# Kernel tuning notes

Hardware: AMD Instinct MI355X
Metric: run time of the kernel (lower is better)

The kernel has to match this reference:

```python
import jax, jax.numpy as jnp
import numpy as np
from jax import lax

K, C, H, W = 5, 256, 64, 64
NH, HD, P = 8, 32, 16           # heads, head_dim, patch_number
H0, W0 = 512, 512               # original mask resolution
SCALE_BASE = HD ** (-0.5)
GN_EPS = 1e-5


def _l2norm(x):
    n = jnp.sqrt(jnp.sum(x * x, axis=-1, keepdims=True))
    return x / jnp.maximum(n, 1e-12)


def _conv(x, w, b, pad):
    y = lax.conv_general_dilated(x, w, (1, 1), [(pad, pad), (pad, pad)],
                                 dimension_numbers=('NCHW', 'OIHW', 'NCHW'))
    return y + b[None, :, None, None]


def _group_norm(x, scale, bias, groups=4):
    n, c, h, w = x.shape
    xg = x.reshape(n, groups, -1)
    mu = jnp.mean(xg, axis=-1, keepdims=True)
    var = jnp.var(xg, axis=-1, keepdims=True)
    xg = (xg - mu) / jnp.sqrt(var + GN_EPS)
    return xg.reshape(n, c, h, w) * scale[None, :, None, None] + bias[None, :, None, None]


def setup_inputs() -> dict:
    key = jax.random.key(0)
    ks = jax.random.split(key, 16)
    x = jax.random.normal(ks[0], (1 + K, C, H, W), dtype=jnp.float32)
    delta = (jax.random.uniform(ks[1], (K, 1, H0, W0)) < 0.3).astype(jnp.float32)
    w = lambda k, sh: jax.random.normal(k, sh, dtype=jnp.float32) * 0.02
    return {
        'x': x, 'delta_onehot_x': delta,
        'Wq': w(ks[2], (C, C)), 'bq': jnp.zeros((C,), jnp.float32),
        'Ws': w(ks[3], (C, C)), 'bs': jnp.zeros((C,), jnp.float32),
        'scale': jnp.array(1.0, jnp.float32),
        'c1w': w(ks[4], (16, NH, 5, 5)), 'c1b': jnp.zeros((16,), jnp.float32),
        'g1s': jnp.ones((16,), jnp.float32), 'g1b': jnp.zeros((16,), jnp.float32),
        'c2w': w(ks[5], (64, 16, 3, 3)), 'c2b': jnp.zeros((64,), jnp.float32),
        'g2s': jnp.ones((64,), jnp.float32), 'g2b': jnp.zeros((64,), jnp.float32),
        'c3w': w(ks[6], (128, 64, 3, 3)), 'c3b': jnp.zeros((128,), jnp.float32),
        'g3s': jnp.ones((128,), jnp.float32), 'g3b': jnp.zeros((128,), jnp.float32),
    }


def reference(x, delta_onehot_x, Wq, bq, Ws, bs, scale,
              c1w, c1b, g1s, g1b, c2w, c2b, g2s, g2b, c3w, c3b, g3s, g3b):
    q = jnp.transpose(x[:1], (0, 2, 3, 1))    # [1,H,W,C]
    s = jnp.transpose(x[1:], (0, 2, 3, 1))    # [K,H,W,C]

    # nearest interpolation (torch 'nearest': src = floor(dst*in/out))
    ih = (jnp.arange(H) * H0) // H
    iw = (jnp.arange(W) * W0) // W
    d = delta_onehot_x[:, :, ih][:, :, :, iw]  # [K,1,H,W]

    q = (q @ Wq.T + bq).reshape(H, W, NH, HD).transpose(2, 0, 1, 3)        # [h,H,W,d]
    s = (s @ Ws.T + bs).reshape(K, H, W, NH, HD).transpose(0, 3, 1, 2, 4)  # [K,h,H,W,d]
    q = _l2norm(q) * scale * SCALE_BASE
    s = _l2norm(s)

    Hp, Wp = H // P, W // P
    S = P * P
    fg = d.reshape(K, P, Hp, P, Wp).transpose(0, 1, 3, 2, 4).reshape(K, S, Hp * Wp)
    bg = 1.0 - fg
    fg_sum = jnp.sum(fg, axis=-1)  # [K,S]
    bg_sum = jnp.sum(bg, axis=-1)

    sp = s.reshape(K, NH, P, Hp, P, Wp, HD).transpose(0, 1, 2, 4, 3, 5, 6)
    sp = sp.reshape(K, NH, S, Hp * Wp, HD)

    cs_fg = _l2norm(jnp.einsum('ksl,khsld->khsd', fg, sp))
    cs_bg = _l2norm(jnp.einsum('ksl,khsld->khsd', bg, sp))
    c_s = jnp.concatenate([cs_fg, cs_bg], axis=2).transpose(1, 0, 2, 3).reshape(NH, K * 2 * S, HD)
    c_v = jnp.concatenate([jnp.ones((K, NH, S), q.dtype), jnp.zeros((K, NH, S), q.dtype)],
                          axis=2).transpose(1, 0, 2).reshape(NH, K * 2 * S)

    mask = jnp.concatenate([jnp.where(fg_sum < 1.0, -jnp.inf, 0.0),
                            jnp.where(bg_sum < 1.0, -jnp.inf, 0.0)], axis=1)  # [K,2S]
    mask = mask.reshape(1, 1, 1, -1)

    attn = jax.nn.softmax(jnp.einsum('hyxd,hsd->hyxs', q, c_s) + mask, axis=-1)
    xo = jnp.einsum('hyxs,hs->hyx', attn, c_v)[None]  # [1,h,H,W]

    out = jax.nn.relu(_group_norm(_conv(xo, c1w, c1b, 2), g1s, g1b))
    out = jax.nn.relu(_group_norm(_conv(out, c2w, c2b, 1), g2s, g2b))
    out = jax.nn.relu(_group_norm(_conv(out, c3w, c3b, 1), g3s, g3b))
    return out
```

## Files before the change

### kernel.cpp

```cpp
#include <hip/hip_runtime.h>
#include <hip/hip_bf16.h>
#include <cstddef>

#define HW 4096

typedef __attribute__((ext_vector_type(8))) short bf16x8;
typedef __attribute__((ext_vector_type(4))) float f32x4;

__device__ __forceinline__ unsigned short f2b(float v) {
  __hip_bfloat16 b = __float2bfloat16(v);
  return *reinterpret_cast<unsigned short*>(&b);
}
__device__ __forceinline__ float b2f(unsigned short u) {
  return __bfloat162float(*reinterpret_cast<const __hip_bfloat16*>(&u));
}

__global__ __launch_bounds__(256) void txp_kernel(const float* __restrict__ x,
                                                  unsigned short* __restrict__ xb) {
  const int n = blockIdx.z, p0 = blockIdx.x * 64, ci0 = blockIdx.y * 64;
  const int t = threadIdx.x;
  __shared__ float Tl[64][65];
#pragma unroll
  for (int pass = 0; pass < 16; ++pass) {
    int ci = pass * 4 + (t >> 6), px = t & 63;
    Tl[ci][px] = x[((size_t)n * 256 + ci0 + ci) * HW + p0 + px];
  }
  __syncthreads();
#pragma unroll
  for (int pass = 0; pass < 16; ++pass) {
    int px = pass * 4 + (t >> 6), ci = t & 63;
    xb[((size_t)n * HW + p0 + px) * 256 + ci0 + ci] = f2b(Tl[ci][px]);
  }
}

__global__ __launch_bounds__(256) void wcv_kernel(const float* __restrict__ Wq,
                                                  const float* __restrict__ Ws,
                                                  unsigned short* __restrict__ wb) {
  int i = blockIdx.x * 256 + threadIdx.x;
  const float* W = (i < 65536) ? Wq : Ws;
  wb[i] = f2b(W[i & 65535]);
}

__global__ __launch_bounds__(256) void proj_kernel(
    const unsigned short* __restrict__ xb, const unsigned short* __restrict__ wb,
    const float* __restrict__ bq, const float* __restrict__ bs,
    const float* __restrict__ scale,
    unsigned short* __restrict__ qb, unsigned short* __restrict__ sb) {
  const int row0 = blockIdx.x * 128;
  const int n    = row0 >> 12;
  const int co0  = blockIdx.y * 64;
  const int t    = threadIdx.x;
  const int wv   = t >> 6;
  const int l    = t & 63;
  const float* __restrict__ B = (n == 0) ? bq : bs;
  const unsigned short* __restrict__ Wb = wb + (size_t)(n == 0 ? 0 : 1) * 65536;
  const int prow = row0 + wv * 32;

  const size_t ar0 = ((size_t)prow + (l & 15)) * 256 + (l >> 4) * 8;
  const size_t ar1 = ar0 + 16 * 256;
  size_t br[4];
#pragma unroll
  for (int b = 0; b < 4; ++b)
    br[b] = ((size_t)(co0 + b * 16 + (l & 15))) * 256 + (l >> 4) * 8;

  f32x4 acc[2][4];
#pragma unroll
  for (int a = 0; a < 2; ++a)
#pragma unroll
    for (int b = 0; b < 4; ++b) acc[a][b] = (f32x4){0.f, 0.f, 0.f, 0.f};

#pragma unroll
  for (int kc = 0; kc < 8; ++kc) {
    bf16x8 a0 = *(const bf16x8*)&xb[ar0 + kc * 32];
    bf16x8 a1 = *(const bf16x8*)&xb[ar1 + kc * 32];
#pragma unroll
    for (int b = 0; b < 4; ++b) {
      bf16x8 bb = *(const bf16x8*)&Wb[br[b] + kc * 32];
      acc[0][b] = __builtin_amdgcn_mfma_f32_16x16x32_bf16(a0, bb, acc[0][b], 0, 0, 0);
      acc[1][b] = __builtin_amdgcn_mfma_f32_16x16x32_bf16(a1, bb, acc[1][b], 0, 0, 0);
    }
  }

  float bias[4];
#pragma unroll
  for (int b = 0; b < 4; ++b) bias[b] = B[co0 + b * 16 + (l & 15)];
  const float qsc = scale[0] * 0.17677669529663687f;

#pragma unroll
  for (int a = 0; a < 2; ++a) {
#pragma unroll
    for (int r = 0; r < 4; ++r) {
      float v0 = acc[a][0][r] + bias[0];
      float v1 = acc[a][1][r] + bias[1];
      float v2 = acc[a][2][r] + bias[2];
      float v3 = acc[a][3][r] + bias[3];
      float s0 = v0 * v0 + v1 * v1;
      float s1 = v2 * v2 + v3 * v3;
#pragma unroll
      for (int m = 1; m <= 8; m <<= 1) {
        s0 += __shfl_xor(s0, m);
        s1 += __shfl_xor(s1, m);
      }
      float n0 = fmaxf(sqrtf(s0), 1e-12f);
      float n1 = fmaxf(sqrtf(s1), 1e-12f);
      v0 /= n0; v1 /= n0; v2 /= n1; v3 /= n1;
      const int px = prow + a * 16 + (l >> 4) * 4 + r;
      if (n == 0) {
        size_t o = (size_t)px * 256 + co0 + (l & 15);
        qb[o +  0] = f2b(v0 * qsc);
        qb[o + 16] = f2b(v1 * qsc);
        qb[o + 32] = f2b(v2 * qsc);
        qb[o + 48] = f2b(v3 * qsc);
      } else {
        size_t o = ((size_t)(px - 4096 * 1) + (size_t)(n - 1) * HW - (size_t)(n - 1) * HW) * 0;
        size_t so = ((size_t)(px - 4096) ) * 256 + co0 + (l & 15);
        sb[so +  0] = f2b(v0);
        sb[so + 16] = f2b(v1);
        sb[so + 32] = f2b(v2);
        sb[so + 48] = f2b(v3);
      }
    }
  }
}

__global__ __launch_bounds__(256) void agg_kernel(
    const float* __restrict__ delta, const unsigned short* __restrict__ sb,
    unsigned short* __restrict__ cb, float* __restrict__ mask) {
  const int s = blockIdx.x;
  const int k = blockIdx.y;
  const int t = threadIdx.x;
  __shared__ float fgl[16];
  const int sy = (s >> 4) * 4, sx = (s & 15) * 4;
  if (t < 16) {
    int y0 = (sy + (t >> 2)) * 8, x0 = (sx + (t & 3)) * 8;
    fgl[t] = delta[(size_t)k * 512 * 512 + (size_t)y0 * 512 + x0];
  }
  __syncthreads();
  const int h = t >> 5, d = t & 31;
  float af = 0.f, ab = 0.f;
#pragma unroll
  for (int l = 0; l < 16; ++l) {
    int pix = (sy + (l >> 2)) * 64 + sx + (l & 3);
    float sv = b2f(sb[((size_t)k * HW + pix) * 256 + h * 32 + d]);
    float f = fgl[l];
    af += f * sv;
    ab += (1.f - f) * sv;
  }
  float ssf = af * af, ssb = ab * ab;
#pragma unroll
  for (int m = 1; m <= 16; m <<= 1) {
    ssf += __shfl_xor(ssf, m);
    ssb += __shfl_xor(ssb, m);
  }
  float vf = af / fmaxf(sqrtf(ssf), 1e-12f);
  float vb = ab / fmaxf(sqrtf(ssb), 1e-12f);
  const int jf = k * 512 + s, jb = jf + 256;
  cb[((size_t)h * 2560 + jf) * 32 + d] = f2b(vf);
  cb[((size_t)h * 2560 + jb) * 32 + d] = f2b(vb);
  if (t == 0) {
    float fs = 0.f;
#pragma unroll
    for (int l = 0; l < 16; ++l) fs += fgl[l];
    mask[jf] = (fs < 1.f) ? -1e30f : 0.f;
    mask[jb] = ((16.f - fs) < 1.f) ? -1e30f : 0.f;
  }
}

__global__ __launch_bounds__(256) void attn_kernel(
    const unsigned short* __restrict__ qb, const unsigned short* __restrict__ cb,
    const float* __restrict__ mask, float* __restrict__ xo) {
  const int t = threadIdx.x;
  const int wv = t >> 6;
  const int l = t & 63;
  const int h = blockIdx.y;
  const int p0 = blockIdx.x * 64 + wv * 16;

  __shared__ float ml[2560];
  for (int i = t; i < 2560; i += 256) ml[i] = mask[i];

  const bf16x8 a = *(const bf16x8*)&qb[(size_t)(p0 + (l & 15)) * 256 + h * 32 + (l >> 4) * 8];
  __syncthreads();

  float num[4] = {0.f, 0.f, 0.f, 0.f}, den[4] = {0.f, 0.f, 0.f, 0.f};
  const size_t cbase = (size_t)h * 2560 * 32 + ((size_t)(l >> 4)) * 8;

  for (int j0 = 0; j0 < 2560; j0 += 16) {
    bf16x8 b = *(const bf16x8*)&cb[cbase + (size_t)(j0 + (l & 15)) * 32];
    f32x4 dacc = {0.f, 0.f, 0.f, 0.f};
    dacc = __builtin_amdgcn_mfma_f32_16x16x32_bf16(a, b, dacc, 0, 0, 0);
    float m = ml[j0 + (l & 15)];
    float cv = ((j0 & 511) < 256) ? 1.f : 0.f;
#pragma unroll
    for (int r = 0; r < 4; ++r) {
      float e = __expf(dacc[r] + m);
      den[r] += e;
      num[r] += cv * e;
    }
  }

#pragma unroll
  for (int r = 0; r < 4; ++r) {
#pragma unroll
    for (int msk = 1; msk <= 8; msk <<= 1) {
      den[r] += __shfl_xor(den[r], msk);
      num[r] += __shfl_xor(num[r], msk);
    }
  }
  if ((l & 15) == 0) {
#pragma unroll
    for (int r = 0; r < 4; ++r) {
      int px = p0 + (l >> 4) * 4 + r;
      xo[(size_t)h * HW + px] = num[r] / den[r];
    }
  }
}

template <int CIC, int KS, int PAD, int COT>
__global__ __launch_bounds__(256) void conv_split(
    const float* __restrict__ in, const float* __restrict__ w,
    float* __restrict__ pp, int CI) {
  constexpr int R = 4 + KS - 1;
  constexpr int C = 64 + 2 * PAD;
  const int t   = threadIdx.x;
  const int y0  = blockIdx.x * 4;
  const int co0 = blockIdx.y * COT;
  const int cb0 = blockIdx.z * CIC;
  const int CO  = gridDim.y * COT;

  __shared__ float Xl[CIC][R][C];
  __shared__ float Wl[CIC][KS * KS][COT];

  const int xi = t & 63;
  const int yr = t >> 6;

  float acc[COT];
#pragma unroll
  for (int c = 0; c < COT; ++c) acc[c] = 0.f;

  for (int idx = t; idx < CIC * R * C; idx += 256) {
    int ci = idx / (R * C), rem = idx % (R * C), pr = rem / C, pc = rem % C;
    int iy = y0 + pr - PAD, ix = pc - PAD;
    float v = 0.f;
    if (iy >= 0 && iy < 64 && ix >= 0 && ix < 64)
      v = in[(size_t)(cb0 + ci) * HW + iy * 64 + ix];
    Xl[ci][pr][pc] = v;
  }
  for (int idx = t; idx < CIC * KS * KS * COT; idx += 256) {
    int ci = idx / (KS * KS * COT), rem = idx % (KS * KS * COT);
    int kk = rem / COT, c = rem % COT;
    Wl[ci][kk][c] = w[(size_t)((co0 + c) * CI + cb0 + ci) * KS * KS + kk];
  }
  __syncthreads();

#pragma unroll
  for (int ci = 0; ci < CIC; ++ci)
#pragma unroll
    for (int ky = 0; ky < KS; ++ky)
#pragma unroll
      for (int kx = 0; kx < KS; ++kx) {
        float xv = Xl[ci][yr + ky][xi + kx];
        if constexpr (COT % 4 == 0) {
          const float4* w4 = (const float4*)&Wl[ci][ky * KS + kx][0];
#pragma unroll
          for (int c4 = 0; c4 < COT / 4; ++c4) {
            float4 wv = w4[c4];
            acc[c4 * 4 + 0] += xv * wv.x;
            acc[c4 * 4 + 1] += xv * wv.y;
            acc[c4 * 4 + 2] += xv * wv.z;
            acc[c4 * 4 + 3] += xv * wv.w;
          }
        } else {
#pragma unroll
          for (int c = 0; c < COT; ++c) acc[c] += xv * Wl[ci][ky * KS + kx][c];
        }
      }

  const int p = (y0 + yr) * 64 + xi;
  float* o = pp + (size_t)blockIdx.z * CO * HW;
#pragma unroll
  for (int c = 0; c < COT; ++c)
    o[(size_t)(co0 + c) * HW + p] = acc[c];
}

__global__ __launch_bounds__(256) void merge_stats(
    const float* __restrict__ pp, const float* __restrict__ b,
    float* __restrict__ out, float* __restrict__ stp, int S, int CO) {
  __shared__ float sh[256], sh2[256];
  const int t = threadIdx.x;
  const int idx = blockIdx.x * 256 + t;
  const int c = idx >> 12;
  float v = b[c];
  const size_t stride = (size_t)CO * HW;
  for (int s = 0; s < S; ++s) v += pp[(size_t)s * stride + idx];
  out[idx] = v;
  sh[t] = v; sh2[t] = v * v;
  __syncthreads();
  for (int w = 128; w > 0; w >>= 1) {
    if (t < w) { sh[t] += sh[t + w]; sh2[t] += sh2[t + w]; }
    __syncthreads();
  }
  if (t == 0) { stp[blockIdx.x * 2] = sh[0]; stp[blockIdx.x * 2 + 1] = sh2[0]; }
}

__global__ __launch_bounds__(256) void gn_apply(
    const float* __restrict__ in, float* __restrict__ out, const float* __restrict__ stp,
    const float* __restrict__ gs, const float* __restrict__ gb, int cpg, int bpg) {
  __shared__ float sh[256], sh2[256];
  const int t = threadIdx.x;
  const int idx = blockIdx.x * 256 + t;
  const int c = idx >> 12;
  const int g = c / cpg;
  float s = 0.f, ss = 0.f;
  for (int i = t; i < bpg; i += 256) {
    s  += stp[(g * bpg + i) * 2];
    ss += stp[(g * bpg + i) * 2 + 1];
  }
  sh[t] = s; sh2[t] = ss;
  __syncthreads();
  for (int w = 128; w > 0; w >>= 1) {
    if (t < w) { sh[t] += sh[t + w]; sh2[t] += sh2[t + w]; }
    __syncthreads();
  }
  const float nn = (float)(cpg * HW);
  const float mean = sh[0] / nn;
  const float var = sh2[0] / nn - mean * mean;
  const float rstd = 1.0f / sqrtf(var + 1e-5f);
  float v = (in[idx] - mean) * rstd * gs[c] + gb[c];
  out[idx] = fmaxf(v, 0.f);
}

extern "C" void kernel_launch(void* const* d_in, const int* in_sizes, int n_in,
                              void* d_out, int out_size, void* d_ws, size_t ws_size,
                              hipStream_t stream) {
  const float* x     = (const float*)d_in[0];
  const float* delta = (const float*)d_in[1];
  const float* Wq    = (const float*)d_in[2];
  const float* bq    = (const float*)d_in[3];
  const float* Ws    = (const float*)d_in[4];
  const float* bs    = (const float*)d_in[5];
  const float* scale = (const float*)d_in[6];
  const float* c1w = (const float*)d_in[7],  *c1b = (const float*)d_in[8];
  const float* g1s = (const float*)d_in[9],  *g1b = (const float*)d_in[10];
  const float* c2w = (const float*)d_in[11], *c2b = (const float*)d_in[12];
  const float* g2s = (const float*)d_in[13], *g2b = (const float*)d_in[14];
  const float* c3w = (const float*)d_in[15], *c3b = (const float*)d_in[16];
  const float* g3s = (const float*)d_in[17], *g3b = (const float*)d_in[18];

  float* ws = (float*)d_ws;
  unsigned short* sb = (unsigned short*)ws;
  unsigned short* xb = (unsigned short*)(ws + 2621440);
  unsigned short* qb = (unsigned short*)(ws + 5767168);
  unsigned short* cb = (unsigned short*)(ws + 6291456);
  float* mask = ws + 6619136;
  float* xo   = mask + 2560;
  float* stp  = xo + 32768;
  unsigned short* wb = (unsigned short*)(stp + 4096);
  float* pp = ws;
  float* t1 = ws + 2097152;
  float* a1 = t1 + 65536;
  float* t2 = a1 + 65536;
  float* a2 = t2 + 262144;
  float* t3 = a2 + 262144;

  txp_kernel<<<dim3(64, 4, 6), 256, 0, stream>>>(x, xb);
  wcv_kernel<<<512, 256, 0, stream>>>(Wq, Ws, wb);
  proj_kernel<<<dim3(192, 4), 256, 0, stream>>>(xb, wb, bq, bs, scale, qb, sb);
  agg_kernel<<<dim3(256, 5), 256, 0, stream>>>(delta, sb, cb, mask);
  attn_kernel<<<dim3(64, 8), 256, 0, stream>>>(qb, cb, mask, xo);

  conv_split<4, 5, 2, 2><<<dim3(16, 8, 2), 256, 0, stream>>>(xo, c1w, pp, 8);
  merge_stats<<<256, 256, 0, stream>>>(pp, c1b, t1, stp, 2, 16);
  gn_apply<<<256, 256, 0, stream>>>(t1, a1, stp, g1s, g1b, 4, 64);

  conv_split<8, 3, 1, 4><<<dim3(16, 16, 2), 256, 0, stream>>>(a1, c2w, pp, 16);
  merge_stats<<<1024, 256, 0, stream>>>(pp, c2b, t2, stp, 2, 64);
  gn_apply<<<1024, 256, 0, stream>>>(t2, a2, stp, g2s, g2b, 16, 256);

  conv_split<16, 3, 1, 8><<<dim3(16, 16, 4), 256, 0, stream>>>(a2, c3w, pp, 64);
  merge_stats<<<2048, 256, 0, stream>>>(pp, c3b, t3, stp, 4, 128);
  gn_apply<<<2048, 256, 0, stream>>>(t3, (float*)d_out, stp, g3s, g3b, 32, 512);
}
```

Baseline: 124.6 us.

## Fuse conv bias, GroupNorm stats and GN-apply into conv kernels

Replaces the split-K conv, merge_stats and gn_apply chain for the first two conv layers with fused kernels. Each conv now adds bias and writes per-block partial sums for the GroupNorm statistics. The next conv reduces those partials, then applies GN and ReLU while loading its input tile. This drops four kernel launches and the intermediate normalized-activation round trips. In exchange the conv1 and conv2 grids lose the input-channel split parallelism, and variance is now computed as E[x^2]-mean^2 from partial sums.

```diff
diff --git a/kernel.cpp b/kernel.cpp
--- a/kernel.cpp
+++ b/kernel.cpp
@@ -112,8 +112,7 @@
         qb[o + 32] = f2b(v2 * qsc);
         qb[o + 48] = f2b(v3 * qsc);
       } else {
-        size_t o = ((size_t)(px - 4096 * 1) + (size_t)(n - 1) * HW - (size_t)(n - 1) * HW) * 0;
-        size_t so = ((size_t)(px - 4096) ) * 256 + co0 + (l & 15);
+        size_t so = ((size_t)(px - 4096)) * 256 + co0 + (l & 15);
         sb[so +  0] = f2b(v0);
         sb[so + 16] = f2b(v1);
         sb[so + 32] = f2b(v2);
@@ -215,70 +214,187 @@
   }
 }
 
-template <int CIC, int KS, int PAD, int COT>
-__global__ __launch_bounds__(256) void conv_split(
+__global__ __launch_bounds__(256) void conv1_stats(
     const float* __restrict__ in, const float* __restrict__ w,
-    float* __restrict__ pp, int CI) {
-  constexpr int R = 4 + KS - 1;
-  constexpr int C = 64 + 2 * PAD;
-  const int t   = threadIdx.x;
-  const int y0  = blockIdx.x * 4;
-  const int co0 = blockIdx.y * COT;
-  const int cb0 = blockIdx.z * CIC;
-  const int CO  = gridDim.y * COT;
-
-  __shared__ float Xl[CIC][R][C];
-  __shared__ float Wl[CIC][KS * KS][COT];
-
-  const int xi = t & 63;
-  const int yr = t >> 6;
-
-  float acc[COT];
-#pragma unroll
-  for (int c = 0; c < COT; ++c) acc[c] = 0.f;
-
-  for (int idx = t; idx < CIC * R * C; idx += 256) {
-    int ci = idx / (R * C), rem = idx % (R * C), pr = rem / C, pc = rem % C;
-    int iy = y0 + pr - PAD, ix = pc - PAD;
+    const float* __restrict__ b, float* __restrict__ out, float* __restrict__ stp) {
+  const int t = threadIdx.x;
+  const int y0 = blockIdx.x * 2;
+  const int co0 = blockIdx.y * 2;
+  __shared__ float Xl[8][6][68];
+  __shared__ float Wl[8][25][2];
+  __shared__ float sh[256], sh2[256];
+
+  for (int idx = t; idx < 8 * 6 * 68; idx += 256) {
+    int ci = idx / 408, rem = idx % 408, pr = rem / 68, pc = rem % 68;
+    int iy = y0 + pr - 2, ix = pc - 2;
     float v = 0.f;
-    if (iy >= 0 && iy < 64 && ix >= 0 && ix < 64)
-      v = in[(size_t)(cb0 + ci) * HW + iy * 64 + ix];
+    if (iy >= 0 && iy < 64 && ix >= 0 && ix < 64) v = in[(size_t)ci * HW + iy * 64 + ix];
     Xl[ci][pr][pc] = v;
   }
-  for (int idx = t; idx < CIC * KS * KS * COT; idx += 256) {
-    int ci = idx / (KS * KS * COT), rem = idx % (KS * KS * COT);
-    int kk = rem / COT, c = rem % COT;
-    Wl[ci][kk][c] = w[(size_t)((co0 + c) * CI + cb0 + ci) * KS * KS + kk];
-  }
-  __syncthreads();
-
-#pragma unroll
-  for (int ci = 0; ci < CIC; ++ci)
-#pragma unroll
-    for (int ky = 0; ky < KS; ++ky)
-#pragma unroll
-      for (int kx = 0; kx < KS; ++kx) {
+  for (int idx = t; idx < 400; idx += 256) {
+    int ci = idx / 50, rem = idx % 50, kk = rem / 2, c = rem % 2;
+    Wl[ci][kk][c] = w[(size_t)((co0 + c) * 8 + ci) * 25 + kk];
+  }
+  __syncthreads();
+
+  const int co_s = t >> 7, yr = (t >> 6) & 1, xi = t & 63;
+  float acc = b[co0 + co_s];
+#pragma unroll
+  for (int ci = 0; ci < 8; ++ci)
+#pragma unroll
+    for (int ky = 0; ky < 5; ++ky)
+#pragma unroll
+      for (int kx = 0; kx < 5; ++kx)
+        acc += Xl[ci][yr + ky][xi + kx] * Wl[ci][ky * 5 + kx][co_s];
+  out[(size_t)(co0 + co_s) * HW + (y0 + yr) * 64 + xi] = acc;
+
+  sh[t] = acc; sh2[t] = acc * acc;
+  __syncthreads();
+  for (int w2 = 128; w2 > 0; w2 >>= 1) {
+    if (t < w2) { sh[t] += sh[t + w2]; sh2[t] += sh2[t + w2]; }
+    __syncthreads();
+  }
+  if (t == 0) {
+    int bid = blockIdx.y * 32 + blockIdx.x;
+    stp[bid * 2] = sh[0]; stp[bid * 2 + 1] = sh2[0];
+  }
+}
+
+__global__ __launch_bounds__(256) void conv2_gn(
+    const float* __restrict__ t1, const float* __restrict__ stp1,
+    const float* __restrict__ g1s, const float* __restrict__ g1b,
+    const float* __restrict__ w, const float* __restrict__ b,
+    float* __restrict__ t2, float* __restrict__ stp2) {
+  const int t = threadIdx.x;
+  const int y0 = blockIdx.x * 4;
+  const int co0 = blockIdx.y * 4;
+  __shared__ float Xl[16][6][66];
+  __shared__ float Wl[16][9][4];
+  __shared__ float gstat[4][2];
+  __shared__ float sh[256], sh2[256];
+
+  {
+    int g = t >> 6, i = t & 63;
+    float s = stp1[(g * 64 + i) * 2], ss = stp1[(g * 64 + i) * 2 + 1];
+#pragma unroll
+    for (int m = 1; m <= 32; m <<= 1) { s += __shfl_xor(s, m); ss += __shfl_xor(ss, m); }
+    if (i == 0) {
+      float nn = 4.f * HW;
+      float mean = s / nn, var = ss / nn - mean * mean;
+      gstat[g][0] = mean;
+      gstat[g][1] = 1.f / sqrtf(var + 1e-5f);
+    }
+  }
+  __syncthreads();
+
+  for (int idx = t; idx < 16 * 6 * 66; idx += 256) {
+    int ci = idx / 396, rem = idx % 396, pr = rem / 66, pc = rem % 66;
+    int iy = y0 + pr - 1, ix = pc - 1;
+    float v = 0.f;
+    if (iy >= 0 && iy < 64 && ix >= 0 && ix < 64) {
+      float raw = t1[(size_t)ci * HW + iy * 64 + ix];
+      v = fmaxf((raw - gstat[ci >> 2][0]) * gstat[ci >> 2][1] * g1s[ci] + g1b[ci], 0.f);
+    }
+    Xl[ci][pr][pc] = v;
+  }
+  for (int idx = t; idx < 16 * 9 * 4; idx += 256) {
+    int ci = idx / 36, rem = idx % 36, kk = rem / 4, c = rem % 4;
+    Wl[ci][kk][c] = w[(size_t)((co0 + c) * 16 + ci) * 9 + kk];
+  }
+  __syncthreads();
+
+  const int xi = t & 63, yr = t >> 6;
+  float acc[4] = {b[co0], b[co0 + 1], b[co0 + 2], b[co0 + 3]};
+#pragma unroll
+  for (int ci = 0; ci < 16; ++ci)
+#pragma unroll
+    for (int ky = 0; ky < 3; ++ky)
+#pragma unroll
+      for (int kx = 0; kx < 3; ++kx) {
         float xv = Xl[ci][yr + ky][xi + kx];
-        if constexpr (COT % 4 == 0) {
-          const float4* w4 = (const float4*)&Wl[ci][ky * KS + kx][0];
-#pragma unroll
-          for (int c4 = 0; c4 < COT / 4; ++c4) {
-            float4 wv = w4[c4];
-            acc[c4 * 4 + 0] += xv * wv.x;
-            acc[c4 * 4 + 1] += xv * wv.y;
-            acc[c4 * 4 + 2] += xv * wv.z;
-            acc[c4 * 4 + 3] += xv * wv.w;
-          }
-        } else {
-#pragma unroll
-          for (int c = 0; c < COT; ++c) acc[c] += xv * Wl[ci][ky * KS + kx][c];
-        }
+        float4 wv = *(const float4*)&Wl[ci][ky * 3 + kx][0];
+        acc[0] += xv * wv.x; acc[1] += xv * wv.y;
+        acc[2] += xv * wv.z; acc[3] += xv * wv.w;
       }
-
   const int p = (y0 + yr) * 64 + xi;
-  float* o = pp + (size_t)blockIdx.z * CO * HW;
-#pragma unroll
-  for (int c = 0; c < COT; ++c)
+  float s = 0.f, ss = 0.f;
+#pragma unroll
+  for (int c = 0; c < 4; ++c) {
+    t2[(size_t)(co0 + c) * HW + p] = acc[c];
+    s += acc[c]; ss += acc[c] * acc[c];
+  }
+  sh[t] = s; sh2[t] = ss;
+  __syncthreads();
+  for (int w2 = 128; w2 > 0; w2 >>= 1) {
+    if (t < w2) { sh[t] += sh[t + w2]; sh2[t] += sh2[t + w2]; }
+    __syncthreads();
+  }
+  if (t == 0) {
+    int bid = blockIdx.y * 16 + blockIdx.x;
+    stp2[bid * 2] = sh[0]; stp2[bid * 2 + 1] = sh2[0];
+  }
+}
+
+__global__ __launch_bounds__(256) void conv3_gn(
+    const float* __restrict__ t2, const float* __restrict__ stp2,
+    const float* __restrict__ g2s, const float* __restrict__ g2b,
+    const float* __restrict__ w, float* __restrict__ pp) {
+  const int t = threadIdx.x;
+  const int y0 = blockIdx.x * 4;
+  const int co0 = blockIdx.y * 8;
+  const int z = blockIdx.z;
+  const int cb0 = z * 16;
+  __shared__ float Xl[16][6][66];
+  __shared__ float Wl[16][9][8];
+  __shared__ float gm, gr;
+
+  if (t < 64) {
+    float s = stp2[(z * 64 + t) * 2], ss = stp2[(z * 64 + t) * 2 + 1];
+#pragma unroll
+    for (int m = 1; m <= 32; m <<= 1) { s += __shfl_xor(s, m); ss += __shfl_xor(ss, m); }
+    if (t == 0) {
+      float nn = 16.f * HW;
+      float mean = s / nn, var = ss / nn - mean * mean;
+      gm = mean;
+      gr = 1.f / sqrtf(var + 1e-5f);
+    }
+  }
+  __syncthreads();
+
+  for (int idx = t; idx < 16 * 6 * 66; idx += 256) {
+    int ci = idx / 396, rem = idx % 396, pr = rem / 66, pc = rem % 66;
+    int iy = y0 + pr - 1, ix = pc - 1;
+    float v = 0.f;
+    if (iy >= 0 && iy < 64 && ix >= 0 && ix < 64) {
+      float raw = t2[(size_t)(cb0 + ci) * HW + iy * 64 + ix];
+      v = fmaxf((raw - gm) * gr * g2s[cb0 + ci] + g2b[cb0 + ci], 0.f);
+    }
+    Xl[ci][pr][pc] = v;
+  }
+  for (int idx = t; idx < 16 * 9 * 8; idx += 256) {
+    int ci = idx / 72, rem = idx % 72, kk = rem / 8, c = rem % 8;
+    Wl[ci][kk][c] = w[(size_t)((co0 + c) * 64 + cb0 + ci) * 9 + kk];
+  }
+  __syncthreads();
+
+  const int xi = t & 63, yr = t >> 6;
+  float acc[8] = {0.f, 0.f, 0.f, 0.f, 0.f, 0.f, 0.f, 0.f};
+#pragma unroll
+  for (int ci = 0; ci < 16; ++ci)
+#pragma unroll
+    for (int ky = 0; ky < 3; ++ky)
+#pragma unroll
+      for (int kx = 0; kx < 3; ++kx) {
+        float xv = Xl[ci][yr + ky][xi + kx];
+        const float4* w4 = (const float4*)&Wl[ci][ky * 3 + kx][0];
+        float4 w0 = w4[0], w1 = w4[1];
+        acc[0] += xv * w0.x; acc[1] += xv * w0.y; acc[2] += xv * w0.z; acc[3] += xv * w0.w;
+        acc[4] += xv * w1.x; acc[5] += xv * w1.y; acc[6] += xv * w1.z; acc[7] += xv * w1.w;
+      }
+  const int p = (y0 + yr) * 64 + xi;
+  float* o = pp + (size_t)z * 128 * HW;
+#pragma unroll
+  for (int c = 0; c < 8; ++c)
     o[(size_t)(co0 + c) * HW + p] = acc[c];
 }
 
@@ -353,14 +469,14 @@
   unsigned short* cb = (unsigned short*)(ws + 6291456);
   float* mask = ws + 6619136;
   float* xo   = mask + 2560;
-  float* stp  = xo + 32768;
-  unsigned short* wb = (unsigned short*)(stp + 4096);
+  float* stp1 = xo + 32768;
+  float* stp2 = stp1 + 512;
+  float* stp3 = stp2 + 512;
+  unsigned short* wb = (unsigned short*)(stp3 + 4096);
   float* pp = ws;
   float* t1 = ws + 2097152;
-  float* a1 = t1 + 65536;
-  float* t2 = a1 + 65536;
-  float* a2 = t2 + 262144;
-  float* t3 = a2 + 262144;
+  float* t2 = t1 + 65536;
+  float* t3 = t2 + 262144;
 
   txp_kernel<<<dim3(64, 4, 6), 256, 0, stream>>>(x, xb);
   wcv_kernel<<<512, 256, 0, stream>>>(Wq, Ws, wb);
@@ -368,15 +484,9 @@
   agg_kernel<<<dim3(256, 5), 256, 0, stream>>>(delta, sb, cb, mask);
   attn_kernel<<<dim3(64, 8), 256, 0, stream>>>(qb, cb, mask, xo);
 
-  conv_split<4, 5, 2, 2><<<dim3(16, 8, 2), 256, 0, stream>>>(xo, c1w, pp, 8);
-  merge_stats<<<256, 256, 0, stream>>>(pp, c1b, t1, stp, 2, 16);
-  gn_apply<<<256, 256, 0, stream>>>(t1, a1, stp, g1s, g1b, 4, 64);
-
-  conv_split<8, 3, 1, 4><<<dim3(16, 16, 2), 256, 0, stream>>>(a1, c2w, pp, 16);
-  merge_stats<<<1024, 256, 0, stream>>>(pp, c2b, t2, stp, 2, 64);
-  gn_apply<<<1024, 256, 0, stream>>>(t2, a2, stp, g2s, g2b, 16, 256);
-
-  conv_split<16, 3, 1, 8><<<dim3(16, 16, 4), 256, 0, stream>>>(a2, c3w, pp, 64);
-  merge_stats<<<2048, 256, 0, stream>>>(pp, c3b, t3, stp, 4, 128);
-  gn_apply<<<2048, 256, 0, stream>>>(t3, (float*)d_out, stp, g3s, g3b, 32, 512);
-}
+  conv1_stats<<<dim3(32, 8), 256, 0, stream>>>(xo, c1w, c1b, t1, stp1);
+  conv2_gn<<<dim3(16, 16), 256, 0, stream>>>(t1, stp1, g1s, g1b, c2w, c2b, t2, stp2);
+  conv3_gn<<<dim3(16, 16, 4), 256, 0, stream>>>(t2, stp2, g2s, g2b, c3w, pp);
+  merge_stats<<<2048, 256, 0, stream>>>(pp, c3b, t3, stp3, 4, 128);
+  gn_apply<<<2048, 256, 0, stream>>>(t3, (float*)d_out, stp3, g3s, g3b, 32, 512);
+}
```

Result: slower. 127.6 us (+2.4%).
